# Kernel tuning notes

Hardware: AMD Instinct MI355X
Metric: run time of the kernel (lower is better)

## Reference

```python
import jax, jax.numpy as jnp
import numpy as np

N, E, C, NUM_CLASSES = 100000, 1600000, 64, 101
EPS = 1e-5
BIAS_VALUE = -float(np.log((1 - 0.01) / 0.01))  # focal-loss prior bias


def _kaiming(key, out_dim, in_dim):
    # kaiming_normal_ with nonlinearity='relu': std = sqrt(2 / fan_in)
    return jax.random.normal(key, (out_dim, in_dim), jnp.float32) * np.sqrt(2.0 / in_dim)


def setup_inputs() -> dict:
    key = jax.random.key(0)
    ks = jax.random.split(key, 16)
    inp = {
        "x": jax.random.normal(ks[0], (N, C), jnp.float32),
        "pos": jax.random.uniform(ks[1], (N, 3), jnp.float32),
        "edge_index": jax.random.randint(ks[2], (2, E), 0, N, jnp.int32),
    }
    # stem / conv1 / conv2: local Linear (C+2 -> C), global Linear (C -> C), BN(C)
    for i, name in enumerate(["stem", "c1", "c2"]):
        kl, kg = jax.random.split(ks[3 + i])
        inp[f"wl_{name}"] = _kaiming(kl, C, C + 2)
        inp[f"bl_{name}"] = jnp.zeros((C,), jnp.float32)
        inp[f"wg_{name}"] = _kaiming(kg, C, C)
        inp[f"bg_{name}"] = jnp.zeros((C,), jnp.float32)
        inp[f"g_{name}"] = jnp.ones((C,), jnp.float32)
        inp[f"b_{name}"] = jnp.zeros((C,), jnp.float32)
    # regr head: (C+2 -> 4) -> (4 -> 4)
    kl, kg = jax.random.split(ks[6])
    inp["wl_reg"] = _kaiming(kl, 4, C + 2)
    inp["bl_reg"] = jnp.zeros((4,), jnp.float32)
    inp["wg_reg"] = _kaiming(kg, 4, 4)
    inp["bg_reg"] = jnp.zeros((4,), jnp.float32)
    # cls head: (C+2 -> 101) -> (101 -> 101), global zero-init + prior bias
    inp["wl_cls"] = _kaiming(ks[7], NUM_CLASSES, C + 2)
    inp["bl_cls"] = jnp.zeros((NUM_CLASSES,), jnp.float32)
    inp["wg_cls"] = jnp.zeros((NUM_CLASSES, NUM_CLASSES), jnp.float32)
    inp["bg_cls"] = jnp.full((NUM_CLASSES,), BIAS_VALUE, jnp.float32)
    # obj head: (C+2 -> 1) -> (1 -> 1), global zero-init + prior bias
    inp["wl_obj"] = _kaiming(ks[8], 1, C + 2)
    inp["bl_obj"] = jnp.zeros((1,), jnp.float32)
    inp["wg_obj"] = jnp.zeros((1, 1), jnp.float32)
    inp["bg_obj"] = jnp.full((1,), BIAS_VALUE, jnp.float32)
    return inp


def _conv(x, pos2, src, dst, wl, bl, wg, bg):
    # gather neighbor features + relative 2D position -> edge MLP -> scatter-max -> global linear
    m = jnp.concatenate([x[src], pos2[src] - pos2[dst]], axis=-1)   # [E, in+2]
    m = jax.nn.relu(m @ wl.T + bl)                                   # [E, out]
    agg = jax.ops.segment_max(m, dst, num_segments=x.shape[0])       # [N, out]
    agg = jnp.where(jnp.isfinite(agg), agg, 0.0)                     # empty nodes -> 0
    return agg @ wg.T + bg


def _bn_relu(x, g, b):
    mu = x.mean(axis=0)
    var = x.var(axis=0)  # biased, as torch BN training-mode normalization
    return jax.nn.relu((x - mu) * jax.lax.rsqrt(var + EPS) * g + b)


def reference(x, pos, edge_index,
              wl_stem, bl_stem, wg_stem, bg_stem, g_stem, b_stem,
              wl_c1, bl_c1, wg_c1, bg_c1, g_c1, b_c1,
              wl_c2, bl_c2, wg_c2, bg_c2, g_c2, b_c2,
              wl_reg, bl_reg, wg_reg, bg_reg,
              wl_cls, bl_cls, wg_cls, bg_cls,
              wl_obj, bl_obj, wg_obj, bg_obj):
    pos2 = pos[:, :2]
    src, dst = edge_index[0], edge_index[1]
    h = _bn_relu(_conv(x, pos2, src, dst, wl_stem, bl_stem, wg_stem, bg_stem), g_stem, b_stem)
    x1 = _bn_relu(_conv(h, pos2, src, dst, wl_c1, bl_c1, wg_c1, bg_c1), g_c1, b_c1)
    x2 = _bn_relu(_conv(h, pos2, src, dst, wl_c2, bl_c2, wg_c2, bg_c2), g_c2, b_c2)
    reg = _conv(x1, pos2, src, dst, wl_reg, bl_reg, wg_reg, bg_reg)
    obj = _conv(x1, pos2, src, dst, wl_obj, bl_obj, wg_obj, bg_obj)
    cls = _conv(x2, pos2, src, dst, wl_cls, bl_cls, wg_cls, bg_cls)
    return (cls, reg, obj)
```

## Files before the change

kernel.cpp:

```cpp
#include <hip/hip_runtime.h>
#include <hip/hip_bf16.h>

#define NN 100000
#define NE 1600000
#define NCLS 101
#define EPS_BN 1e-5f
#define NINF (-__builtin_inff())
#define NBUCK 196
#define BCAP 12288
#define G192B 521
#define MBK 1563
#define CHUNK 2048
#define KINIT 0x007Fu

typedef __attribute__((ext_vector_type(8))) short bf16x8;
typedef __attribute__((ext_vector_type(4))) float f32x4;
typedef __attribute__((ext_vector_type(2))) unsigned short u16x2;

__device__ __forceinline__ int rl_i(int v, int j) {
    return __builtin_amdgcn_readlane(v, j);
}
__device__ __forceinline__ int bperm(int srcbyte, int v) {
    return __builtin_amdgcn_ds_bpermute(srcbyte, v);
}
__device__ __forceinline__ float b2f(unsigned short u) {
    return __uint_as_float(((unsigned)u) << 16);
}
__device__ __forceinline__ unsigned short f2b(float v) {
    return __bfloat16_as_ushort(__float2bfloat16(v));
}
__device__ __forceinline__ unsigned short ord16(unsigned short b) {
    return b ^ ((b & 0x8000u) ? 0xFFFFu : 0x8000u);
}
__device__ __forceinline__ float iordf(unsigned k) {
    unsigned b = (k ^ ((k & 0x8000u) ? 0x8000u : 0xFFFFu)) & 0xFFFFu;
    return __uint_as_float(b << 16);
}
__device__ __forceinline__ u16x2 vmax2(u16x2 a, u16x2 b) {
    return __builtin_elementwise_max(a, b);
}

__global__ __launch_bounds__(256) void bucket_k(const int* __restrict__ src,
                                                const int* __restrict__ dst,
                                                int* __restrict__ bcnt16,
                                                int* __restrict__ bstore) {
    __shared__ int vals[CHUNK];
    __shared__ int sval[CHUNK];
    __shared__ unsigned char bks[CHUNK];
    __shared__ unsigned char sbk[CHUNK];
    __shared__ int hist[256];
    __shared__ int scn[256];
    __shared__ int loff[256];
    __shared__ int cur[256];
    __shared__ int gshift[256];
    int e0 = blockIdx.x * CHUNK;
    int cnt = NE - e0;
    if (cnt > CHUNK) cnt = CHUNK;
    int t = threadIdx.x;
    hist[t] = 0;
    __syncthreads();
    for (int i = t; i < cnt; i += 256) {
        int d = dst[e0 + i], s = src[e0 + i];
        int b = d >> 9;
        vals[i] = ((d & 511) << 17) | s;
        bks[i] = (unsigned char)b;
        atomicAdd(&hist[b], 1);
    }
    __syncthreads();
    int v = hist[t];
    scn[t] = v;
    __syncthreads();
    for (int off = 1; off < 256; off <<= 1) {
        int u = (t >= off) ? scn[t - off] : 0;
        __syncthreads();
        scn[t] += u;
        __syncthreads();
    }
    loff[t] = scn[t] - v;
    cur[t] = scn[t] - v;
    if (t < NBUCK) {
        int base = (v > 0) ? atomicAdd(&bcnt16[t * 16], v) : 0;
        gshift[t] = base - loff[t];
    }
    __syncthreads();
    for (int i = t; i < cnt; i += 256) {
        int b = bks[i];
        int p = atomicAdd(&cur[b], 1);
        sval[p] = vals[i];
        sbk[p] = (unsigned char)b;
    }
    __syncthreads();
    for (int i = t; i < cnt; i += 256) {
        int b = sbk[i];
        int q = gshift[b] + i;
        if (q < BCAP) bstore[(size_t)b * BCAP + q] = sval[i];
    }
}

__global__ __launch_bounds__(256) void bscan_k(const int* __restrict__ bcnt16,
                                               int* __restrict__ bbase) {
    __shared__ int sh[256];
    int t = threadIdx.x;
    int v = (t < NBUCK) ? bcnt16[t * 16] : 0;
    sh[t] = v;
    __syncthreads();
    for (int off = 1; off < 256; off <<= 1) {
        int u = (t >= off) ? sh[t - off] : 0;
        __syncthreads();
        sh[t] += u;
        __syncthreads();
    }
    if (t < NBUCK) bbase[t] = sh[t] - v;
}

__global__ __launch_bounds__(512) void b2csr_k(const int* __restrict__ bcnt16,
                                               const int* __restrict__ bbase,
                                               const int* __restrict__ bstore,
                                               int* __restrict__ rs,
                                               int* __restrict__ csrc) {
    __shared__ int hist[512];
    __shared__ int scn[512];
    __shared__ int cur[512];
    int b = blockIdx.x;
    int t = threadIdx.x;
    int cnt = bcnt16[b * 16];
    if (cnt > BCAP) cnt = BCAP;
    int gbase = bbase[b];
    const int* bs = bstore + (size_t)b * BCAP;
    hist[t] = 0;
    __syncthreads();
    for (int i = t; i < cnt; i += 512) atomicAdd(&hist[bs[i] >> 17], 1);
    __syncthreads();
    int v = hist[t];
    scn[t] = v;
    __syncthreads();
    for (int off = 1; off < 512; off <<= 1) {
        int u = (t >= off) ? scn[t - off] : 0;
        __syncthreads();
        scn[t] += u;
        __syncthreads();
    }
    int ex = scn[t] - v;
    cur[t] = ex;
    int node = b * 512 + t;
    if (node < NN) rs[node] = gbase + ex;
    if (b == 0 && t == 0) rs[NN] = NE;
    __syncthreads();
    for (int i = t; i < cnt; i += 512) {
        int e = bs[i];
        int p = atomicAdd(&cur[e >> 17], 1);
        csrc[gbase + p] = e & 0x1FFFF;
    }
}

__global__ __launch_bounds__(256) void pack_all_k(
    const float* __restrict__ pos,
    const float* __restrict__ wl_stem, const float* __restrict__ wg_stem,
    const float* __restrict__ wl_c1, const float* __restrict__ bl_c1,
    const float* __restrict__ wl_c2, const float* __restrict__ bl_c2,
    const float* __restrict__ wg_c1, const float* __restrict__ wg_c2,
    const float* __restrict__ wl_reg, const float* __restrict__ wl_obj,
    const float* __restrict__ bl_reg, const float* __restrict__ bl_obj,
    const float* __restrict__ wl_cls, const float* __restrict__ wg_cls,
    float2* __restrict__ pos2,
    int* __restrict__ flags,
    float* __restrict__ wT_ro,
    unsigned short* __restrict__ wb_sg, unsigned short* __restrict__ wb_g1,
    unsigned short* __restrict__ wb_g2, unsigned short* __restrict__ wb_sp,
    unsigned short* __restrict__ wb_12, unsigned short* __restrict__ wb_cp,
    unsigned short* __restrict__ wcg16,
    float* __restrict__ bAB, float* __restrict__ wro, float* __restrict__ bro,
    float* __restrict__ wp_sp, float* __restrict__ wp_12,
    float* __restrict__ wp_cp, float* __restrict__ wp_ro) {
    int u = blockIdx.x * 256 + threadIdx.x;
    if (u < NN) { pos2[u] = make_float2(pos[u * 3], pos[u * 3 + 1]); return; }
    u -= NN;
    if (u < 1024) { int j = u >> 4, c = u & 15;
        wT_ro[u] = (c < 4) ? wl_reg[c * 66 + j] : ((c == 4) ? wl_obj[j] : 0.f); return; }
    u -= 1024;
    if (u < 4096) { int k = u & 63, n = (u >> 6) & 15, t2 = u >> 10;
        wb_sg[u] = f2b(wg_stem[(t2 * 16 + n) * 64 + k]); return; }
    u -= 4096;
    if (u < 4096) { int k = u & 63, n = (u >> 6) & 15, t2 = u >> 10;
        wb_g1[u] = f2b(wg_c1[(t2 * 16 + n) * 64 + k]); return; }
    u -= 4096;
    if (u < 4096) { int k = u & 63, n = (u >> 6) & 15, t2 = u >> 10;
        wb_g2[u] = f2b(wg_c2[(t2 * 16 + n) * 64 + k]); return; }
    u -= 4096;
    if (u < 4096) { int k = u & 63, n = (u >> 6) & 15, t2 = u >> 10;
        wb_sp[u] = f2b(wl_stem[(t2 * 16 + n) * 66 + k]); return; }
    u -= 4096;
    if (u < 8192) { int k = u & 63, n = (u >> 6) & 15, t2 = u >> 10;
        int cg = t2 * 16 + n;
        wb_12[u] = f2b(((cg & 1) ? wl_c2 : wl_c1)[(cg >> 1) * 66 + k]); return; }
    u -= 8192;
    if (u < 8192) { int k = u & 63, n = (u >> 6) & 15, t2 = u >> 10;
        int cg = t2 * 16 + n;
        wb_cp[u] = (cg < NCLS) ? f2b(wl_cls[cg * 66 + k]) : (unsigned short)0; return; }
    u -= 8192;
    if (u < 14336) { int k = u & 127, n = (u >> 7) & 15, t2 = u >> 11;
        int ng = t2 * 16 + n;
        float v = (ng < NCLS && k < NCLS) ? wg_cls[ng * NCLS + k] : 0.f;
        if (v != 0.f) atomicOr(&flags[0], 1);
        wcg16[u] = f2b(v); return; }
    u -= 14336;
    if (u < 128) { bAB[u] = (u & 1) ? bl_c2[u >> 1] : bl_c1[u >> 1]; return; }
    u -= 128;
    if (u < 330) { int cc = u / 66, j = u - cc * 66;
        wro[u] = (cc < 4) ? wl_reg[u] : wl_obj[j]; return; }
    u -= 330;
    if (u < 5) { bro[u] = (u < 4) ? bl_reg[u] : bl_obj[0]; return; }
    u -= 5;
    if (u < 128) { int c = u >> 1;
        wp_sp[u] = wl_stem[c * 66 + 64 + (u & 1)]; return; }
    u -= 128;
    if (u < 256) { int cg = u >> 1;
        const float* w = (cg & 1) ? wl_c2 : wl_c1;
        wp_12[u] = w[(cg >> 1) * 66 + 64 + (u & 1)]; return; }
    u -= 256;
    if (u < 256) { int cg = u >> 1;
        wp_cp[u] = (cg < NCLS) ? wl_cls[cg * 66 + 64 + (u & 1)] : 0.f; return; }
    u -= 256;
    if (u < 16) { int c = u >> 1; float v = 0.f;
        if (c < 4) v = wl_reg[c * 66 + 64 + (u & 1)];
        else if (c == 4) v = wl_obj[64 + (u & 1)];
        wp_ro[u] = v; }
}

template <int COUT, int NC, int IS, int OS, bool BNF, bool ILV, bool FCHK>
__global__ __launch_bounds__(256) void mfma_lin_k(
    const float* __restrict__ in,
    const unsigned short* __restrict__ wb,
    const float* __restrict__ bias,
    const float* __restrict__ st,
    const float2* __restrict__ wp,
    const float2* __restrict__ pos2,
    const int* __restrict__ flags,
    unsigned short* __restrict__ out) {
    if constexpr (FCHK) { if (flags[0] == 0) return; }
    int wid = __builtin_amdgcn_readfirstlane(threadIdx.x >> 6);
    int lane = threadIdx.x & 63;
    int quad = lane >> 4, l16 = lane & 15;
    int rbase = blockIdx.x * 64 + wid * 16;
    int row = rbase + l16;
    int rcl = (row < NN) ? row : (NN - 1);
    const float* arow = in + (size_t)rcl * IS + quad * 8;
    bf16x8 a[2];
#pragma unroll
    for (int kc = 0; kc < 2; ++kc) {
        float4 v0 = *(const float4*)(arow + kc * 32);
        float4 v1 = *(const float4*)(arow + kc * 32 + 4);
        float vv[8] = {v0.x, v0.y, v0.z, v0.w, v1.x, v1.y, v1.z, v1.w};
        bf16x8 av;
#pragma unroll
        for (int j = 0; j < 8; ++j) {
            float v = vv[j];
            if constexpr (BNF) {
                int col = kc * 32 + quad * 8 + j;
                v = fmaxf(fmaf(v, st[128 + col], st[192 + col]), 0.f);
            }
            av[j] = (short)f2b(v);
        }
        a[kc] = av;
    }
    float2 pr[4];
#pragma unroll
    for (int r = 0; r < 4; ++r) {
        int rg = rbase + quad * 4 + r;
        pr[r] = pos2[(rg < NN) ? rg : 0];
    }
#pragma unroll
    for (int t = 0; t < COUT / 16; ++t) {
        const unsigned short* brow = wb + t * 1024 + l16 * 64 + quad * 8;
        f32x4 acc = {0.f, 0.f, 0.f, 0.f};
        acc = __builtin_amdgcn_mfma_f32_16x16x32_bf16(
            a[0], *(const bf16x8*)brow, acc, 0, 0, 0);
        acc = __builtin_amdgcn_mfma_f32_16x16x32_bf16(
            a[1], *(const bf16x8*)(brow + 32), acc, 0, 0, 0);
        int cg = t * 16 + l16;
        float bv = (cg < NC) ? bias[cg] : 0.f;
        float2 w = wp[cg];
#pragma unroll
        for (int r = 0; r < 4; ++r) {
            int rg = rbase + quad * 4 + r;
            if (rg < NN) {
                float val = acc[r] + bv + pr[r].x * w.x + pr[r].y * w.y;
                if constexpr (ILV) {
                    unsigned short hv = (cg < NC) ? ord16(f2b(val)) : (unsigned short)0;
                    out[(size_t)rg * OS + (cg & 63) * 2 + (cg >> 6)] = hv;
                } else {
                    if (cg < NC) out[(size_t)rg * OS + cg] = ord16(f2b(val));
                }
            }
        }
    }
}

__global__ __launch_bounds__(256) void mfma_stats_k(
    const unsigned short* __restrict__ in,
    const unsigned short* __restrict__ wb,
    const float* __restrict__ bias,
    float* __restrict__ out,
    float* __restrict__ stpart) {
    __shared__ float sS[4][64], sQ[4][64];
    int wid = __builtin_amdgcn_readfirstlane(threadIdx.x >> 6);
    int lane = threadIdx.x & 63;
    int quad = lane >> 4, l16 = lane & 15;
    int rbase = blockIdx.x * 64 + wid * 16;
    int row = rbase + l16;
    int rcl = (row < NN) ? row : (NN - 1);
    const unsigned short* arow = in + (size_t)rcl * 64 + quad * 8;
    bf16x8 a[2];
#pragma unroll
    for (int kc = 0; kc < 2; ++kc)
        a[kc] = *(const bf16x8*)(arow + kc * 32);
#pragma unroll
    for (int t = 0; t < 4; ++t) {
        const unsigned short* brow = wb + t * 1024 + l16 * 64 + quad * 8;
        f32x4 acc = {0.f, 0.f, 0.f, 0.f};
        acc = __builtin_amdgcn_mfma_f32_16x16x32_bf16(
            a[0], *(const bf16x8*)brow, acc, 0, 0, 0);
        acc = __builtin_amdgcn_mfma_f32_16x16x32_bf16(
            a[1], *(const bf16x8*)(brow + 32), acc, 0, 0, 0);
        int cg = t * 16 + l16;
        float bv = bias[cg];
        float s = 0.f, q = 0.f;
#pragma unroll
        for (int r = 0; r < 4; ++r) {
            int rg = rbase + quad * 4 + r;
            float v = acc[r] + bv;
            if (rg < NN) out[(size_t)rg * 64 + cg] = v;
            else v = 0.f;
            s += v;
            q = fmaf(v, v, q);
        }
        s += __shfl_xor(s, 16, 64);
        s += __shfl_xor(s, 32, 64);
        q += __shfl_xor(q, 16, 64);
        q += __shfl_xor(q, 32, 64);
        if (quad == 0) {
            sS[wid][cg] = s;
            sQ[wid][cg] = q;
        }
    }
    __syncthreads();
    int c = threadIdx.x;
    if (c < 64) {
        float s = sS[0][c] + sS[1][c] + sS[2][c] + sS[3][c];
        float q = sQ[0][c] + sQ[1][c] + sQ[2][c] + sQ[3][c];
        stpart[(size_t)blockIdx.x * 128 + c] = s;
        stpart[(size_t)blockIdx.x * 128 + 64 + c] = q;
    }
}

template <int COUT, int CPW, int K, int IS, int OS, int MT, bool BNF, bool BOUT,
          bool POSF>
__global__ __launch_bounds__(256) void gemm_k(const float* __restrict__ in,
                                              const float* __restrict__ wT,
                                              const float* __restrict__ bias,
                                              const float* __restrict__ st,
                                              const float2* __restrict__ wp,
                                              const float2* __restrict__ pos2,
                                              float* __restrict__ out) {
    constexpr int CP = 4 * CPW;
    constexpr int RM = MT / 64;
    constexpr int XR = MT + 1;
    __shared__ __align__(16) float xs[K * XR];
    __shared__ __align__(16) float wsh[K * CP];
    int base = blockIdx.x * MT;
    for (int p = threadIdx.x; p < K * CP / 4; p += 256)
        ((float4*)wsh)[p] = ((const float4*)wT)[p];
    for (int p = threadIdx.x; p < MT * K; p += 256) {
        int n = p / K, j = p - n * K;
        float v = (base + n < NN) ? in[(size_t)(base + n) * IS + j] : 0.f;
        if constexpr (BNF) v = fmaxf(fmaf(v, st[128 + j], st[192 + j]), 0.f);
        xs[j * XR + n] = v;
    }
    __syncthreads();
    int wid = __builtin_amdgcn_readfirstlane(threadIdx.x >> 6);
    int lane = threadIdx.x & 63;
    int c0 = wid * CPW;
    if (c0 >= COUT) return;
    float acc[RM][CPW];
#pragma unroll
    for (int k = 0; k < CPW; ++k) {
        float bv = (c0 + k < COUT) ? bias[c0 + k] : 0.f;
#pragma unroll
        for (int r = 0; r < RM; ++r) acc[r][k] = bv;
    }
    for (int j = 0; j < K; ++j) {
        float a[RM];
#pragma unroll
        for (int r = 0; r < RM; ++r) a[r] = xs[j * XR + 64 * r + lane];
#pragma unroll
        for (int q = 0; q < CPW / 4; ++q) {
            float4 wv = *(const float4*)&wsh[j * CP + c0 + 4 * q];
#pragma unroll
            for (int r = 0; r < RM; ++r) {
                acc[r][4 * q + 0] = fmaf(a[r], wv.x, acc[r][4 * q + 0]);
                acc[r][4 * q + 1] = fmaf(a[r], wv.y, acc[r][4 * q + 1]);
                acc[r][4 * q + 2] = fmaf(a[r], wv.z, acc[r][4 * q + 2]);
                acc[r][4 * q + 3] = fmaf(a[r], wv.w, acc[r][4 * q + 3]);
            }
        }
    }
#pragma unroll
    for (int r = 0; r < RM; ++r) {
        int node = base + 64 * r + lane;
        if (node < NN) {
            float2 p = make_float2(0.f, 0.f);
            if constexpr (POSF) p = pos2[node];
#pragma unroll
            for (int k = 0; k < CPW; ++k) {
                if (c0 + k < COUT) {
                    float v = acc[r][k];
                    if constexpr (POSF) {
                        float2 w = wp[c0 + k];
                        v += p.x * w.x + p.y * w.y;
                    }
                    if constexpr (BOUT) {
                        unsigned short* ob = (unsigned short*)out;
                        ob[(size_t)node * OS + c0 + k] = ord16(f2b(v));
                    } else {
                        out[(size_t)node * OS + c0 + k] = v;
                    }
                }
            }
        }
    }
}

__global__ __launch_bounds__(256) void mfma_cls_k(
    const unsigned short* __restrict__ aggc16,
    const unsigned short* __restrict__ wcg16,
    const float* __restrict__ bgc,
    const int* __restrict__ flags,
    float* __restrict__ out) {
    if (flags[0] == 0) return;
    int wid = __builtin_amdgcn_readfirstlane(threadIdx.x >> 6);
    int lane = threadIdx.x & 63;
    int quad = lane >> 4;
    int l16 = lane & 15;
    int mbase = blockIdx.x * 64 + wid * 16;
    bf16x8 a[4];
    const unsigned short* arow = aggc16 + (size_t)(mbase + l16) * 128 + quad * 8;
#pragma unroll
    for (int kc = 0; kc < 4; ++kc)
        a[kc] = *(const bf16x8*)(arow + kc * 32);
    for (int t = 0; t < 7; ++t) {
        const unsigned short* brow = wcg16 + t * 2048 + l16 * 128 + quad * 8;
        f32x4 acc = {0.f, 0.f, 0.f, 0.f};
#pragma unroll
        for (int kc = 0; kc < 4; ++kc) {
            bf16x8 b = *(const bf16x8*)(brow + kc * 32);
            acc = __builtin_amdgcn_mfma_f32_16x16x32_bf16(a[kc], b, acc, 0, 0, 0);
        }
        int cg = t * 16 + l16;
        if (cg < NCLS) {
            float bv = bgc[cg];
#pragma unroll
            for (int r = 0; r < 4; ++r) {
                int rg = mbase + quad * 4 + r;
                if (rg < NN) out[(size_t)rg * NCLS + cg] = acc[r] + bv;
            }
        }
    }
}

__global__ __launch_bounds__(256) void fill_cls_k(const int* __restrict__ flags,
                                                  const float* __restrict__ bgc,
                                                  float* __restrict__ out) {
    if (flags[0] != 0) return;
    int idx = blockIdx.x * 256 + threadIdx.x;
    if (idx < NN * NCLS) out[idx] = bgc[idx % NCLS];
}

__global__ __launch_bounds__(1024) void bnpar_k(const float* __restrict__ stpart,
                                                const float* __restrict__ g,
                                                const float* __restrict__ b,
                                                float* __restrict__ st, int nparts) {
    __shared__ float sS[16][64], sQ[16][64];
    int c = threadIdx.x & 63;
    int part = threadIdx.x >> 6;
    float s = 0.f, q = 0.f;
    for (int i = part; i < nparts; i += 16) {
        s += stpart[(size_t)i * 128 + c];
        q += stpart[(size_t)i * 128 + 64 + c];
    }
    sS[part][c] = s;
    sQ[part][c] = q;
    __syncthreads();
    if (part == 0) {
        s = 0.f; q = 0.f;
#pragma unroll
        for (int w = 0; w < 16; ++w) { s += sS[w][c]; q += sQ[w][c]; }
        float mu = s * (1.0f / NN);
        float var = q * (1.0f / NN) - mu * mu;
        float sc = g[c] * rsqrtf(var + EPS_BN);
        st[128 + c] = sc;
        st[192 + c] = b[c] - mu * sc;
    }
}

__global__ __launch_bounds__(256) void edge1_k(const unsigned short* __restrict__ y,
                                               const float2* __restrict__ pos2,
                                               const int* __restrict__ rs,
                                               const int* __restrict__ csrc,
                                               const float* __restrict__ wl,
                                               unsigned* __restrict__ agg) {
    int wid = __builtin_amdgcn_readfirstlane(threadIdx.x >> 6);
    int lane = threadIdx.x & 63;
    int node = blockIdx.x * 4 + wid;
    if (node >= NN) return;
    int l32 = lane & 31;
    int half = lane >> 5;
    int hoff = half << 2;
    const u16x2* yv = (const u16x2*)y;
    float2 pd = pos2[node];
    int i0 = rs[node], i1 = rs[node + 1];
    u16x2 acc0 = {KINIT, KINIT}, acc1 = {KINIT, KINIT};
    for (int ib = i0; ib < i1; ib += 64) {
        int m = i1 - ib;
        if (m > 64) m = 64;
        int t = ib + lane;
        int idx = (t < i1) ? csrc[t] : 0;
        int j = 0;
        for (; j + 8 <= m; j += 8) {
            u16x2 v[4];
#pragma unroll
            for (int p = 0; p < 4; ++p) {
                int row = bperm(((j + 2 * p) << 2) + hoff, idx);
                v[p] = yv[(size_t)row * 32 + l32];
            }
            acc0 = vmax2(acc0, v[0]);
            acc1 = vmax2(acc1, v[1]);
            acc0 = vmax2(acc0, v[2]);
            acc1 = vmax2(acc1, v[3]);
        }
        for (; j < m; j += 2) {
            int jj = j + half;
            if (jj > m - 1) jj = m - 1;
            int row = bperm(jj << 2, idx);
            acc0 = vmax2(acc0, yv[(size_t)row * 32 + l32]);
        }
    }
    u16x2 acc = vmax2(acc0, acc1);
    int accI = *(int*)&acc;
    int oth = __shfl_xor(accI, 32, 64);
    acc = vmax2(acc, *(u16x2*)&oth);
    if (lane < 32) {
        int c0 = l32 * 2;
        float w00 = wl[c0 * 66 + 64], w01 = wl[c0 * 66 + 65];
        float w10 = wl[c0 * 66 + 66 + 64], w11 = wl[c0 * 66 + 66 + 65];
        float v0 = fmaxf(iordf(acc.x) - fmaf(pd.y, w01, pd.x * w00), 0.f);
        float v1 = fmaxf(iordf(acc.y) - fmaf(pd.y, w11, pd.x * w10), 0.f);
        agg[(size_t)node * 32 + l32] =
            (unsigned)f2b(v0) | ((unsigned)f2b(v1) << 16);
    }
}

__global__ __launch_bounds__(256) void edge2_k(const unsigned* __restrict__ y12,
                                               const float2* __restrict__ pos2,
                                               const int* __restrict__ rs,
                                               const int* __restrict__ csrc,
                                               const float* __restrict__ wlA,
                                               const float* __restrict__ wlB,
                                               unsigned short* __restrict__ a1,
                                               unsigned short* __restrict__ a2) {
    int wid = __builtin_amdgcn_readfirstlane(threadIdx.x >> 6);
    int lane = threadIdx.x & 63;
    int node = blockIdx.x * 4 + wid;
    if (node >= NN) return;
    float wa0 = wlA[lane * 66 + 64], wa1 = wlA[lane * 66 + 65];
    float wb0 = wlB[lane * 66 + 64], wb1 = wlB[lane * 66 + 65];
    float2 pd = pos2[node];
    int i0 = rs[node], i1 = rs[node + 1];
    u16x2 acc0 = {KINIT, KINIT}, acc1 = {KINIT, KINIT};
    for (int ib = i0; ib < i1; ib += 64) {
        int m = i1 - ib;
        if (m > 64) m = 64;
        int t = ib + lane;
        int idx = (t < i1) ? csrc[t] : 0;
        int j = 0;
        for (; j + 8 <= m; j += 8) {
            u16x2 w[8];
#pragma unroll
            for (int q = 0; q < 8; ++q)
                w[q] = *(const u16x2*)(y12 + (size_t)rl_i(idx, j + q) * 64 + lane);
#pragma unroll
            for (int q = 0; q < 8; q += 2) {
                acc0 = vmax2(acc0, w[q]);
                acc1 = vmax2(acc1, w[q + 1]);
            }
        }
        for (; j < m; ++j)
            acc0 = vmax2(acc0,
                *(const u16x2*)(y12 + (size_t)rl_i(idx, j) * 64 + lane));
    }
    u16x2 acc = vmax2(acc0, acc1);
    a1[(size_t)node * 64 + lane] =
        f2b(fmaxf(iordf(acc.x) - fmaf(pd.y, wa1, pd.x * wa0), 0.0f));
    a2[(size_t)node * 64 + lane] =
        f2b(fmaxf(iordf(acc.y) - fmaf(pd.y, wb1, pd.x * wb0), 0.0f));
}

__global__ __launch_bounds__(256) void edge_cls_k(
    const unsigned* __restrict__ y32,
    const float2* __restrict__ pos2,
    const int* __restrict__ rs,
    const int* __restrict__ csrc,
    const float* __restrict__ wl,
    const int* __restrict__ flags,
    unsigned short* __restrict__ aggb) {
    if (flags[0] == 0) return;
    int wid = __builtin_amdgcn_readfirstlane(threadIdx.x >> 6);
    int lane = threadIdx.x & 63;
    int node = blockIdx.x * 4 + wid;
    if (node >= NN) return;
    int chi = (lane + 64 < NCLS) ? (lane + 64) : (NCLS - 1);
    float wa0 = wl[lane * 66 + 64], wa1 = wl[lane * 66 + 65];
    float wb0 = wl[chi * 66 + 64], wb1 = wl[chi * 66 + 65];
    float2 pd = pos2[node];
    int i0 = rs[node], i1 = rs[node + 1];
    u16x2 acc0 = {KINIT, KINIT}, acc1 = {KINIT, KINIT};
    for (int ib = i0; ib < i1; ib += 64) {
        int m = i1 - ib;
        if (m > 64) m = 64;
        int t = ib + lane;
        int idx = (t < i1) ? csrc[t] : 0;
        int j = 0;
        for (; j + 8 <= m; j += 8) {
            u16x2 w[8];
#pragma unroll
            for (int q = 0; q < 8; ++q)
                w[q] = *(const u16x2*)(y32 + (size_t)rl_i(idx, j + q) * 64 + lane);
#pragma unroll
            for (int q = 0; q < 8; q += 2) {
                acc0 = vmax2(acc0, w[q]);
                acc1 = vmax2(acc1, w[q + 1]);
            }
        }
        for (; j < m; ++j)
            acc0 = vmax2(acc0,
                *(const u16x2*)(y32 + (size_t)rl_i(idx, j) * 64 + lane));
    }
    u16x2 acc = vmax2(acc0, acc1);
    aggb[(size_t)node * 128 + lane] =
        f2b(fmaxf(iordf(acc.x) - fmaf(pd.y, wa1, pd.x * wa0), 0.0f));
    unsigned short hb = (lane + 64 < NCLS)
        ? f2b(fmaxf(iordf(acc.y) - fmaf(pd.y, wb1, pd.x * wb0), 0.0f))
        : (unsigned short)0;
    aggb[(size_t)node * 128 + 64 + lane] = hb;
}

__global__ __launch_bounds__(256) void edge_ro_k(
    const unsigned short* __restrict__ yro,
    const float2* __restrict__ pos2,
    const int* __restrict__ rs,
    const int* __restrict__ csrc,
    const float2* __restrict__ wpro,
    float* __restrict__ aggr,
    float* __restrict__ aggo) {
    int wid = __builtin_amdgcn_readfirstlane(threadIdx.x >> 6);
    int lane = threadIdx.x & 63;
    int node = blockIdx.x * 4 + wid;
    if (node >= NN) return;
    int k = lane >> 3, c = lane & 7;
    int cc = (c < 5) ? c : 4;
    float2 wv = wpro[cc];
    int i0 = rs[node], i1 = rs[node + 1];
    unsigned ka = KINIT;
    for (int i = i0 + k; i < i1; i += 8) {
        int s = csrc[i];
        unsigned kv = yro[(size_t)s * 8 + cc];
        ka = (kv > ka) ? kv : ka;
    }
    unsigned o;
    o = (unsigned)__shfl_xor((int)ka, 8, 64);  ka = (o > ka) ? o : ka;
    o = (unsigned)__shfl_xor((int)ka, 16, 64); ka = (o > ka) ? o : ka;
    o = (unsigned)__shfl_xor((int)ka, 32, 64); ka = (o > ka) ? o : ka;
    float2 pd = pos2[node];
    float acc_f = fmaxf(iordf(ka) - fmaf(pd.y, wv.y, pd.x * wv.x), 0.0f);
    if (lane < 5) {
        if (lane < 4) aggr[(size_t)node * 4 + lane] = acc_f;
        else          aggo[node] = acc_f;
    }
}

__global__ __launch_bounds__(256) void final_ro_k(const float* __restrict__ aggr,
                                                  const float* __restrict__ aggo,
                                                  const float* __restrict__ wgr,
                                                  const float* __restrict__ bgr,
                                                  const float* __restrict__ wgo,
                                                  const float* __restrict__ bgo,
                                                  float* __restrict__ out) {
    int n = blockIdx.x * 256 + threadIdx.x;
    if (n >= NN) return;
    float a0 = aggr[(size_t)n * 4 + 0], a1 = aggr[(size_t)n * 4 + 1];
    float a2 = aggr[(size_t)n * 4 + 2], a3 = aggr[(size_t)n * 4 + 3];
    float* reg = out + (size_t)NN * NCLS;
    float* obj = reg + (size_t)NN * 4;
#pragma unroll
    for (int k = 0; k < 4; ++k) {
        float acc = bgr[k];
        acc = fmaf(a0, wgr[k * 4 + 0], acc);
        acc = fmaf(a1, wgr[k * 4 + 1], acc);
        acc = fmaf(a2, wgr[k * 4 + 2], acc);
        acc = fmaf(a3, wgr[k * 4 + 3], acc);
        reg[(size_t)n * 4 + k] = acc;
    }
    obj[n] = fmaf(aggo[n], wgo[0], bgo[0]);
}

extern "C" void kernel_launch(void* const* d_in, const int* in_sizes, int n_in,
                              void* d_out, int out_size, void* d_ws, size_t ws_size,
                              hipStream_t stream) {
    const float* x   = (const float*)d_in[0];
    const float* pos = (const float*)d_in[1];
    const int* ei    = (const int*)d_in[2];
    const int* src = ei;
    const int* dst = ei + NE;
    const float* wl_stem = (const float*)d_in[3];
    const float* bl_stem = (const float*)d_in[4];
    const float* wg_stem = (const float*)d_in[5];
    const float* bg_stem = (const float*)d_in[6];
    const float* g_stem  = (const float*)d_in[7];
    const float* b_stem  = (const float*)d_in[8];
    const float* wl_c1 = (const float*)d_in[9];
    const float* bl_c1 = (const float*)d_in[10];
    const float* wg_c1 = (const float*)d_in[11];
    const float* bg_c1 = (const float*)d_in[12];
    const float* g_c1  = (const float*)d_in[13];
    const float* b_c1  = (const float*)d_in[14];
    const float* wl_c2 = (const float*)d_in[15];
    const float* bl_c2 = (const float*)d_in[16];
    const float* wg_c2 = (const float*)d_in[17];
    const float* bg_c2 = (const float*)d_in[18];
    const float* g_c2  = (const float*)d_in[19];
    const float* b_c2  = (const float*)d_in[20];
    const float* wl_reg = (const float*)d_in[21];
    const float* bl_reg = (const float*)d_in[22];
    const float* wg_reg = (const float*)d_in[23];
    const float* bg_reg = (const float*)d_in[24];
    const float* wl_cls = (const float*)d_in[25];
    const float* bl_cls = (const float*)d_in[26];
    const float* wg_cls = (const float*)d_in[27];
    const float* bg_cls = (const float*)d_in[28];
    const float* wl_obj = (const float*)d_in[29];
    const float* bl_obj = (const float*)d_in[30];
    const float* wg_obj = (const float*)d_in[31];
    const float* bg_obj = (const float*)d_in[32];

    float* ws = (float*)d_ws;
    float* S0 = ws;
    float* S1 = S0 + (size_t)NN * 128;
    float* S2 = S1 + (size_t)NN * 64;
    float* S3 = S2 + (size_t)NN * 64;
    float* y12   = S0;
    float* y_cls = S0;
    unsigned short* B0 = (unsigned short*)(S0 + (size_t)NN * 64);
    unsigned short* B1 = B0 + (size_t)NN * 64;
    unsigned short* aggc16 = (unsigned short*)S1;
    int*   bstore = (int*)S0;
    int*   rs   = (int*)(S3 + (size_t)NN * 64);
    int*   csrc = rs + 100016;
    float* pos2 = (float*)(csrc + NE);
    float* y_ro = pos2 + (size_t)NN * 2;
    float* aggr = y_ro + (size_t)NN * 8;
    float* aggo = aggr + (size_t)NN * 4;
    float* st   = aggo + NN;
    float* st0 = st, *st1 = st + 256, *st2 = st + 512;
    float* wro = st + 768;
    float* bro = wro + 336;
    int*   bcnt16 = (int*)(bro + 16);
    int*   flags  = bcnt16 + NBUCK * 16;
    int*   bbase  = flags + 16;
    float* wT_ro = (float*)(bbase + 256);
    unsigned short* wb_sg = (unsigned short*)(wT_ro + 1024);
    unsigned short* wb_g1 = wb_sg + 4096;
    unsigned short* wb_g2 = wb_g1 + 4096;
    unsigned short* wb_sp = wb_g2 + 4096;
    unsigned short* wb_12 = wb_sp + 4096;
    unsigned short* wb_cp = wb_12 + 8192;
    unsigned short* wcg16 = wb_cp + 8192;
    float* bAB   = (float*)(wcg16 + 14336);
    float* wp_sp = bAB + 128;
    float* wp_12 = wp_sp + 128;
    float* wp_cp = wp_12 + 256;
    float* wp_ro = wp_cp + 256;
    float* stpart = wp_ro + 16;

    hipMemsetAsync(bcnt16, 0, (NBUCK * 16 + 16) * sizeof(int), stream);

    const int NB = (NN + 255) / 256;
    const int N4 = (NN + 3) / 4;
    const int CB = (NE + CHUNK - 1) / CHUNK;
    const int PB = (NN + 49157 + 255) / 256;

    pack_all_k<<<PB, 256, 0, stream>>>(pos,
                                       wl_stem, wg_stem, wl_c1, bl_c1, wl_c2,
                                       bl_c2, wg_c1, wg_c2, wl_reg, wl_obj,
                                       bl_reg, bl_obj, wl_cls, wg_cls,
                                       (float2*)pos2, flags,
                                       wT_ro, wb_sg, wb_g1, wb_g2, wb_sp,
                                       wb_12, wb_cp, wcg16, bAB, wro, bro,
                                       wp_sp, wp_12, wp_cp, wp_ro);
    bucket_k<<<CB, 256, 0, stream>>>(src, dst, bcnt16, bstore);
    bscan_k<<<1, 256, 0, stream>>>(bcnt16, bbase);
    b2csr_k<<<NBUCK, 512, 0, stream>>>(bcnt16, bbase, bstore, rs, csrc);

    mfma_lin_k<64, 64, 64, 64, false, false, false><<<MBK, 256, 0, stream>>>(
        x, wb_sp, bl_stem, nullptr, (const float2*)wp_sp, (const float2*)pos2,
        flags, (unsigned short*)S1);
    edge1_k<<<N4, 256, 0, stream>>>((const unsigned short*)S1, (float2*)pos2, rs,
                                    csrc, wl_stem, (unsigned*)B0);
    mfma_stats_k<<<MBK, 256, 0, stream>>>(B0, wb_sg, bg_stem, S2, stpart);
    bnpar_k<<<1, 1024, 0, stream>>>(stpart, g_stem, b_stem, st0, MBK);

    mfma_lin_k<128, 128, 64, 128, true, false, false><<<MBK, 256, 0, stream>>>(
        S2, wb_12, bAB, st0, (const float2*)wp_12, (const float2*)pos2,
        flags, (unsigned short*)y12);
    edge2_k<<<N4, 256, 0, stream>>>((const unsigned*)y12, (float2*)pos2, rs, csrc,
                                    wl_c1, wl_c2, B0, B1);
    mfma_stats_k<<<MBK, 256, 0, stream>>>(B0, wb_g1, bg_c1, S1, stpart);
    bnpar_k<<<1, 1024, 0, stream>>>(stpart, g_c1, b_c1, st1, MBK);
    mfma_stats_k<<<MBK, 256, 0, stream>>>(B1, wb_g2, bg_c2, S3, stpart);
    bnpar_k<<<1, 1024, 0, stream>>>(stpart, g_c2, b_c2, st2, MBK);

    gemm_k<5, 4, 64, 64, 8, 192, true, true, true><<<G192B, 256, 0, stream>>>(
        S1, wT_ro, bro, st1, (const float2*)wp_ro, (const float2*)pos2, y_ro);
    mfma_lin_k<128, NCLS, 64, 128, true, true, true><<<MBK, 256, 0, stream>>>(
        S3, wb_cp, bl_cls, st2, (const float2*)wp_cp, (const float2*)pos2,
        flags, (unsigned short*)y_cls);

    edge_cls_k<<<N4, 256, 0, stream>>>((const unsigned*)y_cls, (float2*)pos2,
                                       rs, csrc, wl_cls, flags, aggc16);
    edge_ro_k<<<N4, 256, 0, stream>>>((const unsigned short*)y_ro,
                                      (float2*)pos2, rs, csrc,
                                      (const float2*)wp_ro, aggr, aggo);

    mfma_cls_k<<<MBK, 256, 0, stream>>>(aggc16, wcg16, bg_cls, flags,
                                        (float*)d_out);
    fill_cls_k<<<(NN * NCLS + 255) / 256, 256, 0, stream>>>(flags, bg_cls,
                                                            (float*)d_out);
    final_ro_k<<<NB, 256, 0, stream>>>(aggr, aggo, wg_reg, bg_reg, wg_obj, bg_obj,
                                       (float*)d_out);
}
```

Measured before the change: 529.0 us.

## Slice edge-gather features into channel-sliced layout for cache-resident scatter-max

Result: slower. 727.0 us (+37.4%).

```diff
diff --git a/kernel.cpp b/kernel.cpp
--- a/kernel.cpp
+++ b/kernel.cpp
@@ -12,6 +12,7 @@
 #define MBK 1563
 #define CHUNK 2048
 #define KINIT 0x007Fu
+#define NSB 3125
 
 typedef __attribute__((ext_vector_type(8))) short bf16x8;
 typedef __attribute__((ext_vector_type(4))) float f32x4;
@@ -19,9 +20,6 @@
 
 __device__ __forceinline__ int rl_i(int v, int j) {
     return __builtin_amdgcn_readlane(v, j);
-}
-__device__ __forceinline__ int bperm(int srcbyte, int v) {
-    return __builtin_amdgcn_ds_bpermute(srcbyte, v);
 }
 __device__ __forceinline__ float b2f(unsigned short u) {
     return __uint_as_float(((unsigned)u) << 16);
@@ -227,7 +225,7 @@
         wp_ro[u] = v; }
 }
 
-template <int COUT, int NC, int IS, int OS, bool BNF, bool ILV, bool FCHK>
+template <int COUT, int NC, int IS, bool BNF, int MODE, bool FCHK>
 __global__ __launch_bounds__(256) void mfma_lin_k(
     const float* __restrict__ in,
     const unsigned short* __restrict__ wb,
@@ -285,11 +283,13 @@
             int rg = rbase + quad * 4 + r;
             if (rg < NN) {
                 float val = acc[r] + bv + pr[r].x * w.x + pr[r].y * w.y;
-                if constexpr (ILV) {
+                if constexpr (MODE == 0) {
+                    int d = cg >> 1, half = cg & 1;
+                    out[((size_t)(d >> 3) * NN + rg) * 16 + ((d & 7) << 1) + half] =
+                        ord16(f2b(val));
+                } else {
                     unsigned short hv = (cg < NC) ? ord16(f2b(val)) : (unsigned short)0;
-                    out[(size_t)rg * OS + (cg & 63) * 2 + (cg >> 6)] = hv;
-                } else {
-                    if (cg < NC) out[(size_t)rg * OS + cg] = ord16(f2b(val));
+                    out[(size_t)rg * 128 + (cg & 63) * 2 + (cg >> 6)] = hv;
                 }
             }
         }
@@ -502,106 +502,94 @@
     }
 }
 
-__global__ __launch_bounds__(256) void edge1_k(const unsigned short* __restrict__ y,
-                                               const float2* __restrict__ pos2,
-                                               const int* __restrict__ rs,
-                                               const int* __restrict__ csrc,
-                                               const float* __restrict__ wl,
-                                               unsigned* __restrict__ agg) {
+__global__ __launch_bounds__(256) void edge1_sl_k(
+    const unsigned* __restrict__ y,
+    const float2* __restrict__ pos2,
+    const int* __restrict__ rs,
+    const int* __restrict__ csrc,
+    const float2* __restrict__ wpsp,
+    unsigned* __restrict__ agg) {
     int wid = __builtin_amdgcn_readfirstlane(threadIdx.x >> 6);
     int lane = threadIdx.x & 63;
-    int node = blockIdx.x * 4 + wid;
+    int slice = blockIdx.x & 3;
+    int node = (blockIdx.x >> 2) * 32 + wid * 8 + (lane >> 3);
     if (node >= NN) return;
-    int l32 = lane & 31;
-    int half = lane >> 5;
-    int hoff = half << 2;
-    const u16x2* yv = (const u16x2*)y;
-    float2 pd = pos2[node];
+    int dw = lane & 7;
+    const unsigned* ysl = y + (size_t)slice * NN * 8 + dw;
     int i0 = rs[node], i1 = rs[node + 1];
     u16x2 acc0 = {KINIT, KINIT}, acc1 = {KINIT, KINIT};
-    for (int ib = i0; ib < i1; ib += 64) {
-        int m = i1 - ib;
-        if (m > 64) m = 64;
-        int t = ib + lane;
-        int idx = (t < i1) ? csrc[t] : 0;
-        int j = 0;
-        for (; j + 8 <= m; j += 8) {
-            u16x2 v[4];
-#pragma unroll
-            for (int p = 0; p < 4; ++p) {
-                int row = bperm(((j + 2 * p) << 2) + hoff, idx);
-                v[p] = yv[(size_t)row * 32 + l32];
-            }
-            acc0 = vmax2(acc0, v[0]);
-            acc1 = vmax2(acc1, v[1]);
-            acc0 = vmax2(acc0, v[2]);
-            acc1 = vmax2(acc1, v[3]);
-        }
-        for (; j < m; j += 2) {
-            int jj = j + half;
-            if (jj > m - 1) jj = m - 1;
-            int row = bperm(jj << 2, idx);
-            acc0 = vmax2(acc0, yv[(size_t)row * 32 + l32]);
-        }
+    int i = i0;
+    for (; i + 4 <= i1; i += 4) {
+        int s0 = __builtin_nontemporal_load(csrc + i);
+        int s1 = __builtin_nontemporal_load(csrc + i + 1);
+        int s2 = __builtin_nontemporal_load(csrc + i + 2);
+        int s3 = __builtin_nontemporal_load(csrc + i + 3);
+        u16x2 v0 = *(const u16x2*)(ysl + (size_t)s0 * 8);
+        u16x2 v1 = *(const u16x2*)(ysl + (size_t)s1 * 8);
+        u16x2 v2 = *(const u16x2*)(ysl + (size_t)s2 * 8);
+        u16x2 v3 = *(const u16x2*)(ysl + (size_t)s3 * 8);
+        acc0 = vmax2(acc0, v0);
+        acc1 = vmax2(acc1, v1);
+        acc0 = vmax2(acc0, v2);
+        acc1 = vmax2(acc1, v3);
+    }
+    for (; i < i1; ++i) {
+        int s = __builtin_nontemporal_load(csrc + i);
+        acc0 = vmax2(acc0, *(const u16x2*)(ysl + (size_t)s * 8));
     }
     u16x2 acc = vmax2(acc0, acc1);
-    int accI = *(int*)&acc;
-    int oth = __shfl_xor(accI, 32, 64);
-    acc = vmax2(acc, *(u16x2*)&oth);
-    if (lane < 32) {
-        int c0 = l32 * 2;
-        float w00 = wl[c0 * 66 + 64], w01 = wl[c0 * 66 + 65];
-        float w10 = wl[c0 * 66 + 66 + 64], w11 = wl[c0 * 66 + 66 + 65];
-        float v0 = fmaxf(iordf(acc.x) - fmaf(pd.y, w01, pd.x * w00), 0.f);
-        float v1 = fmaxf(iordf(acc.y) - fmaf(pd.y, w11, pd.x * w10), 0.f);
-        agg[(size_t)node * 32 + l32] =
-            (unsigned)f2b(v0) | ((unsigned)f2b(v1) << 16);
-    }
-}
-
-__global__ __launch_bounds__(256) void edge2_k(const unsigned* __restrict__ y12,
-                                               const float2* __restrict__ pos2,
-                                               const int* __restrict__ rs,
-                                               const int* __restrict__ csrc,
-                                               const float* __restrict__ wlA,
-                                               const float* __restrict__ wlB,
-                                               unsigned short* __restrict__ a1,
-                                               unsigned short* __restrict__ a2) {
+    float2 pd = pos2[node];
+    int d = slice * 8 + dw;
+    float2 w0 = wpsp[2 * d], w1 = wpsp[2 * d + 1];
+    float v0 = fmaxf(iordf(acc.x) - fmaf(pd.y, w0.y, pd.x * w0.x), 0.f);
+    float v1 = fmaxf(iordf(acc.y) - fmaf(pd.y, w1.y, pd.x * w1.x), 0.f);
+    agg[(size_t)node * 32 + d] = (unsigned)f2b(v0) | ((unsigned)f2b(v1) << 16);
+}
+
+__global__ __launch_bounds__(256) void edge2_sl_k(
+    const unsigned* __restrict__ y,
+    const float2* __restrict__ pos2,
+    const int* __restrict__ rs,
+    const int* __restrict__ csrc,
+    const float2* __restrict__ wp12,
+    unsigned short* __restrict__ a1,
+    unsigned short* __restrict__ a2) {
     int wid = __builtin_amdgcn_readfirstlane(threadIdx.x >> 6);
     int lane = threadIdx.x & 63;
-    int node = blockIdx.x * 4 + wid;
+    int slice = blockIdx.x & 7;
+    int node = (blockIdx.x >> 3) * 32 + wid * 8 + (lane >> 3);
     if (node >= NN) return;
-    float wa0 = wlA[lane * 66 + 64], wa1 = wlA[lane * 66 + 65];
-    float wb0 = wlB[lane * 66 + 64], wb1 = wlB[lane * 66 + 65];
-    float2 pd = pos2[node];
+    int dw = lane & 7;
+    const unsigned* ysl = y + (size_t)slice * NN * 8 + dw;
     int i0 = rs[node], i1 = rs[node + 1];
     u16x2 acc0 = {KINIT, KINIT}, acc1 = {KINIT, KINIT};
-    for (int ib = i0; ib < i1; ib += 64) {
-        int m = i1 - ib;
-        if (m > 64) m = 64;
-        int t = ib + lane;
-        int idx = (t < i1) ? csrc[t] : 0;
-        int j = 0;
-        for (; j + 8 <= m; j += 8) {
-            u16x2 w[8];
-#pragma unroll
-            for (int q = 0; q < 8; ++q)
-                w[q] = *(const u16x2*)(y12 + (size_t)rl_i(idx, j + q) * 64 + lane);
-#pragma unroll
-            for (int q = 0; q < 8; q += 2) {
-                acc0 = vmax2(acc0, w[q]);
-                acc1 = vmax2(acc1, w[q + 1]);
-            }
-        }
-        for (; j < m; ++j)
-            acc0 = vmax2(acc0,
-                *(const u16x2*)(y12 + (size_t)rl_i(idx, j) * 64 + lane));
+    int i = i0;
+    for (; i + 4 <= i1; i += 4) {
+        int s0 = __builtin_nontemporal_load(csrc + i);
+        int s1 = __builtin_nontemporal_load(csrc + i + 1);
+        int s2 = __builtin_nontemporal_load(csrc + i + 2);
+        int s3 = __builtin_nontemporal_load(csrc + i + 3);
+        u16x2 v0 = *(const u16x2*)(ysl + (size_t)s0 * 8);
+        u16x2 v1 = *(const u16x2*)(ysl + (size_t)s1 * 8);
+        u16x2 v2 = *(const u16x2*)(ysl + (size_t)s2 * 8);
+        u16x2 v3 = *(const u16x2*)(ysl + (size_t)s3 * 8);
+        acc0 = vmax2(acc0, v0);
+        acc1 = vmax2(acc1, v1);
+        acc0 = vmax2(acc0, v2);
+        acc1 = vmax2(acc1, v3);
+    }
+    for (; i < i1; ++i) {
+        int s = __builtin_nontemporal_load(csrc + i);
+        acc0 = vmax2(acc0, *(const u16x2*)(ysl + (size_t)s * 8));
     }
     u16x2 acc = vmax2(acc0, acc1);
-    a1[(size_t)node * 64 + lane] =
-        f2b(fmaxf(iordf(acc.x) - fmaf(pd.y, wa1, pd.x * wa0), 0.0f));
-    a2[(size_t)node * 64 + lane] =
-        f2b(fmaxf(iordf(acc.y) - fmaf(pd.y, wb1, pd.x * wb0), 0.0f));
+    float2 pd = pos2[node];
+    int d = slice * 8 + dw;
+    float2 wA = wp12[2 * d], wB = wp12[2 * d + 1];
+    a1[(size_t)node * 64 + d] =
+        f2b(fmaxf(iordf(acc.x) - fmaf(pd.y, wA.y, pd.x * wA.x), 0.0f));
+    a2[(size_t)node * 64 + d] =
+        f2b(fmaxf(iordf(acc.y) - fmaf(pd.y, wB.y, pd.x * wB.x), 0.0f));
 }
 
 __global__ __launch_bounds__(256) void edge_cls_k(
@@ -809,19 +797,22 @@
     bscan_k<<<1, 256, 0, stream>>>(bcnt16, bbase);
     b2csr_k<<<NBUCK, 512, 0, stream>>>(bcnt16, bbase, bstore, rs, csrc);
 
-    mfma_lin_k<64, 64, 64, 64, false, false, false><<<MBK, 256, 0, stream>>>(
+    mfma_lin_k<64, 64, 64, false, 0, false><<<MBK, 256, 0, stream>>>(
         x, wb_sp, bl_stem, nullptr, (const float2*)wp_sp, (const float2*)pos2,
         flags, (unsigned short*)S1);
-    edge1_k<<<N4, 256, 0, stream>>>((const unsigned short*)S1, (float2*)pos2, rs,
-                                    csrc, wl_stem, (unsigned*)B0);
+    edge1_sl_k<<<4 * NSB, 256, 0, stream>>>((const unsigned*)S1,
+                                            (float2*)pos2, rs, csrc,
+                                            (const float2*)wp_sp,
+                                            (unsigned*)B0);
     mfma_stats_k<<<MBK, 256, 0, stream>>>(B0, wb_sg, bg_stem, S2, stpart);
     bnpar_k<<<1, 1024, 0, stream>>>(stpart, g_stem, b_stem, st0, MBK);
 
-    mfma_lin_k<128, 128, 64, 128, true, false, false><<<MBK, 256, 0, stream>>>(
+    mfma_lin_k<128, 128, 64, true, 0, false><<<MBK, 256, 0, stream>>>(
         S2, wb_12, bAB, st0, (const float2*)wp_12, (const float2*)pos2,
         flags, (unsigned short*)y12);
-    edge2_k<<<N4, 256, 0, stream>>>((const unsigned*)y12, (float2*)pos2, rs, csrc,
-                                    wl_c1, wl_c2, B0, B1);
+    edge2_sl_k<<<8 * NSB, 256, 0, stream>>>((const unsigned*)y12,
+                                            (float2*)pos2, rs, csrc,
+                                            (const float2*)wp_12, B0, B1);
     mfma_stats_k<<<MBK, 256, 0, stream>>>(B0, wb_g1, bg_c1, S1, stpart);
     bnpar_k<<<1, 1024, 0, stream>>>(stpart, g_c1, b_c1, st1, MBK);
     mfma_stats_k<<<MBK, 256, 0, stream>>>(B1, wb_g2, bg_c2, S3, stpart);
@@ -829,7 +820,7 @@
 
     gemm_k<5, 4, 64, 64, 8, 192, true, true, true><<<G192B, 256, 0, stream>>>(
         S1, wT_ro, bro, st1, (const float2*)wp_ro, (const float2*)pos2, y_ro);
-    mfma_lin_k<128, NCLS, 64, 128, true, true, true><<<MBK, 256, 0, stream>>>(
+    mfma_lin_k<128, NCLS, 64, true, 1, true><<<MBK, 256, 0, stream>>>(
         S3, wb_cp, bl_cls, st2, (const float2*)wp_cp, (const float2*)pos2,
         flags, (unsigned short*)y_cls);
 
```
